# Optimization experiments

Measured on AMD Instinct MI355X. Metric: run time of the kernel, lower is better.

## Reference

```python
import jax, jax.numpy as jnp
import numpy as np

B, I, H, DEPTH = 128, 768, 768, 8        # levels 0 (root) .. 7 (leaves)
NODES = 2 ** DEPTH - 1                    # 255 nodes, heap / level order
EPS = 1e-5                                # torch LayerNorm default


def setup_inputs() -> dict:
    key = jax.random.key(0)
    ks = jax.random.split(key, 8)
    s = 0.02  # xavier-ish scale to keep gates in a sane range
    return {
        "x": jax.random.normal(ks[0], (B, NODES, I), jnp.float32),
        "Wioux": jax.random.normal(ks[1], (DEPTH, 3 * H, I), jnp.float32) * s,
        "b_ioux": jnp.zeros((DEPTH, 3 * H), jnp.float32),
        "Wiouh": jax.random.normal(ks[2], (DEPTH, 3 * H, H), jnp.float32) * s,
        "Wfx": jax.random.normal(ks[3], (DEPTH, H, I), jnp.float32) * s,
        "b_fx": jnp.ones((DEPTH, H), jnp.float32),  # fx.bias init to ones per _init_weights
        "Wfh": jax.random.normal(ks[4], (DEPTH, H, H), jnp.float32) * s,
        "b_fh": jnp.zeros((DEPTH, H), jnp.float32),
        "ln_c_g": jnp.ones((DEPTH, H), jnp.float32),
        "ln_c_b": jnp.zeros((DEPTH, H), jnp.float32),
        "ln_h_g": jnp.ones((DEPTH, H), jnp.float32),
        "ln_h_b": jnp.zeros((DEPTH, H), jnp.float32),
        "Wout": jax.random.normal(ks[5], (H, H), jnp.float32) * s,
        "b_out": jnp.zeros((H,), jnp.float32),
    }


def _ln(v, g, b):
    m = v.mean(-1, keepdims=True)
    var = ((v - m) ** 2).mean(-1, keepdims=True)
    return (v - m) / jnp.sqrt(var + EPS) * g + b


def reference(x, Wioux, b_ioux, Wiouh, Wfx, b_fx, Wfh, b_fh,
              ln_c_g, ln_c_b, ln_h_g, ln_h_b, Wout, b_out):
    """Child-Sum TreeLSTM over a complete binary tree (heap-ordered nodes),
    processed bottom-up level-by-level; depth-l nodes use parameter set l."""
    bsz = x.shape[0]
    h = None
    for l in range(DEPTH - 1, -1, -1):       # leaves -> root
        n = 2 ** l
        xs = x[:, n - 1:2 * n - 1]            # [B, n, I] inputs at level l
        iou = jnp.einsum('bni,gi->bng', xs, Wioux[l]) + b_ioux[l]
        if h is not None:
            ch_h = h.reshape(bsz, n, 2, H)    # two children per node
            iou = iou + jnp.einsum('bnh,gh->bng', ch_h.sum(2), Wiouh[l])
        i_, o_, u_ = jnp.split(iou, 3, axis=-1)
        i_ = jax.nn.sigmoid(i_)
        o_ = jax.nn.sigmoid(o_)
        u_ = jnp.tanh(u_)
        c = i_ * u_
        if h is not None:
            fxo = jnp.einsum('bni,hi->bnh', xs, Wfx[l]) + b_fx[l]
            f = jax.nn.sigmoid(fxo[:, :, None, :]
                               + jnp.einsum('bnkh,gh->bnkg', ch_h, Wfh[l]) + b_fh[l])
            # NOTE: faithful to source: f gates multiply child *hidden* states
            c = c + (f * ch_h).sum(2)
        c = _ln(c, ln_c_g[l], ln_c_b[l])
        h = o_ * jnp.tanh(c)
        h = _ln(h, ln_h_g[l], ln_h_b[l])      # dropout is identity in eval
    h_root = h[:, 0]                          # [B, H]
    return jnp.einsum('bh,gh->bg', h_root, Wout) + b_out + x[:, 0]
```

## Files before the change

kernel.cpp:

```cpp
#include <hip/hip_runtime.h>
#include <hip/hip_bf16.h>


#define Hdim 768

typedef __hip_bfloat16 bf16;
typedef __attribute__((ext_vector_type(8))) short short8;
typedef __attribute__((ext_vector_type(4))) float floatx4;

__device__ inline float b2f(unsigned short u) {
    union { unsigned int i; float f; } v; v.i = ((unsigned int)u) << 16; return v.f;
}
__device__ inline float b2f(bf16 h) { return b2f(*(unsigned short*)&h); }
__device__ inline unsigned short f2bu(float f) {
    bf16 h = __float2bfloat16(f);
    return *(unsigned short*)&h;
}
__device__ inline ushort4 cvt4(float4 v) {
    ushort4 o; o.x = f2bu(v.x); o.y = f2bu(v.y); o.z = f2bu(v.z); o.w = f2bu(v.w);
    return o;
}

__global__ __launch_bounds__(384) void conv_wcat(
    const float* __restrict__ Wioux, const float* __restrict__ Wiouh,
    const float* __restrict__ Wfx, bf16* __restrict__ W_cat)
{
    const int row = blockIdx.x;
    const int l = row / 3072;
    const int g = row % 3072;
    const int t = threadIdx.x;
    const int k2 = t << 2;
    float4 v;
    if (g < 2304) {
        const float* src = (k2 < 768)
            ? Wioux + ((long)l * 2304 + g) * 768 + k2
            : Wiouh + ((long)l * 2304 + g) * 768 + (k2 - 768);
        v = *(const float4*)src;
    } else if (k2 < 768) {
        v = *(const float4*)(Wfx + ((long)l * 768 + (g - 2304)) * 768 + k2);
    } else {
        v = make_float4(0.f, 0.f, 0.f, 0.f);
    }
    ((ushort4*)(W_cat + (long)row * 1536))[t] = cvt4(v);
}

__global__ __launch_bounds__(256) void prep_misc(
    const float* __restrict__ Wfh, const float* __restrict__ Wout,
    const float* __restrict__ b_ioux, const float* __restrict__ b_fx,
    const float* __restrict__ x,
    bf16* __restrict__ Wfh_bf, bf16* __restrict__ Wout_bf,
    float* __restrict__ b_cat, bf16* __restrict__ leafA)
{
    const int id = blockIdx.x;
    const int t = threadIdx.x;
    if (id < 4608) {
        const long i = (long)id * 256 + t;
        ((ushort4*)Wfh_bf)[i] = cvt4(((const float4*)Wfh)[i]);
    } else if (id < 5184) {
        const long i = (long)(id - 4608) * 256 + t;
        ((ushort4*)Wout_bf)[i] = cvt4(((const float4*)Wout)[i]);
    } else if (id < 5280) {
        const int i = (id - 5184) * 256 + t;
        const int l = i / 3072, g = i % 3072;
        b_cat[i] = (g < 2304) ? b_ioux[l * 2304 + g] : b_fx[l * 768 + (g - 2304)];
    } else if (t < 192) {
        const int m = id - 5280;
        const int b = m >> 7, j = m & 127;
        const float* xr = x + ((long)b * 255 + 127 + j) * Hdim;
        ((ushort4*)(leafA + (long)m * Hdim))[t] = cvt4(((const float4*)xr)[t]);
    }
}

struct GemmDesc {
    const bf16* A; int lda;
    const bf16* W; int ldw;
    const float* bias;
    void* C; int ldc; int c_fp32;
    int K; int nxb;
    const float* addv; long add_stride;
};

static inline GemmDesc mkdesc(const bf16* A, int lda, const bf16* W, int ldw,
                              const float* bias, void* C, int ldc, int c_fp32,
                              int K, int nxb, const float* addv, long add_stride) {
    GemmDesc d; d.A = A; d.lda = lda; d.W = W; d.ldw = ldw; d.bias = bias;
    d.C = C; d.ldc = ldc; d.c_fp32 = c_fp32; d.K = K; d.nxb = nxb;
    d.addv = addv; d.add_stride = add_stride; return d;
}

__global__ __launch_bounds__(256) void gemm_dual(GemmDesc da, int na, GemmDesc db)
{
    __shared__ __align__(16) bf16 As[128 * 32];
    __shared__ __align__(16) bf16 Ws[128 * 32];
    int id = blockIdx.x;
    const bool second = (id >= na);
    if (second) id -= na;
    const GemmDesc d = second ? db : da;
    const int bm = id / d.nxb, bn = id % d.nxb;

    const int t = threadIdx.x;
    const int wave = t >> 6, lane = t & 63;
    const long m_blk = (long)bm << 7;
// ... 43 lines not shown
        for (int i = 0; i < 4; i++) {
            af[i]  = *(const short8*)(AsS + (mrow + i * 16 + fm) * 32 + fk);
            bfr[i] = *(const short8*)(WsS + (ncol + i * 16 + fm) * 32 + fk);
        }
#pragma unroll
        for (int i = 0; i < 4; i++)
#pragma unroll
            for (int j = 0; j < 4; j++)
                acc[i][j] = __builtin_amdgcn_mfma_f32_16x16x32_bf16(
                    af[i], bfr[j], acc[i][j], 0, 0, 0);
        __syncthreads();
    }

    const int crow0 = (lane >> 4) << 2;
    const int ccol = lane & 15;
#pragma unroll
    for (int i = 0; i < 4; i++) {
#pragma unroll
        for (int j = 0; j < 4; j++) {
            const long col = n_blk + ncol + j * 16 + ccol;
            const float bv = d.bias ? d.bias[col] : 0.f;
#pragma unroll
            for (int r = 0; r < 4; r++) {
                const long row = m_blk + mrow + i * 16 + crow0 + r;
                float v = acc[i][j][r] + bv;
                if (d.addv) v += d.addv[row * d.add_stride + col];
                if (d.c_fp32) ((float*)d.C)[row * (long)d.ldc + col] = v;
                else ((bf16*)d.C)[row * (long)d.ldc + col] = __float2bfloat16(v);
            }
        }
    }
}

__global__ __launch_bounds__(512, 2) void gemm8_dual(GemmDesc da, int na, GemmDesc db)
{
    __shared__ __align__(16) char smem[131072];

    int id = blockIdx.x;
    int nwg = na;
    bool second = false;
    if (id >= na) { id -= na; nwg = (int)gridDim.x - na; second = true; }
    const GemmDesc d = second ? db : da;
    {
        const int q = nwg >> 3, r = nwg & 7;
        const int x = id & 7, i2 = id >> 3;
        id = (x < r ? x * (q + 1) : r * (q + 1) + (x - r) * q) + i2;
    }
    const int bm = id / d.nxb, bn = id % d.nxb;
    const int tid = threadIdx.x;
    const int w = tid >> 6, lane = tid & 63;
    const long m_blk = (long)bm << 8;
    const long n_blk = (long)bn << 8;
    const int T = d.K >> 6;

    const int colb = (((lane & 7) ^ ((lane >> 3) & 7)) << 4);
    const int rw = (w << 4) + (lane >> 3);
    const long ldaB = (long)d.lda * 2, ldwB = (long)d.ldw * 2;
    const char* gA0 = (const char*)(d.A + m_blk * d.lda) + (long)rw * ldaB + colb;
    const char* gB0 = (const char*)(d.W + n_blk * d.ldw) + (long)rw * ldwB + colb;
    const long aH = ldaB << 7, bH = ldwB << 7;
    const long a8 = ldaB << 3, b8 = ldwB << 3;
    char* lW = smem + (w << 11);

    auto stageA = [&](int tile, int buf, int half) {
        const char* g = gA0 + (half ? aH : 0) + ((long)tile << 7);
        char* l = lW + buf * 32768 + half * 16384;
        __builtin_amdgcn_global_load_lds(
            (const __attribute__((address_space(1))) unsigned int*)g,
            (__attribute__((address_space(3))) unsigned int*)l, 16, 0, 0);
        __builtin_amdgcn_global_load_lds(
            (const __attribute__((address_space(1))) unsigned int*)(g + a8),
            (__attribute__((address_space(3))) unsigned int*)(l + 1024), 16, 0, 0);
    };
    auto stageB = [&](int tile, int buf, int half) {
        const char* g = gB0 + (half ? bH : 0) + ((long)tile << 7);
        char* l = lW + 65536 + buf * 32768 + half * 16384;
        __builtin_amdgcn_global_load_lds(
            (const __attribute__((address_space(1))) unsigned int*)g,
            (__attribute__((address_space(3))) unsigned int*)l, 16, 0, 0);
        __builtin_amdgcn_global_load_lds(
            (const __attribute__((address_space(1))) unsigned int*)(g + b8),
            (__attribute__((address_space(3))) unsigned int*)(l + 1024), 16, 0, 0);
    };

    const int fm = lane & 15;
    const int fkB = (lane >> 4) << 4;
    const int sx = (lane & 7) << 4;
    const int cx0 = fkB ^ sx;
    const int cx1 = cx0 ^ 64;
    const int arow0 = ((w >> 2) << 7) + fm;
    const int brow0 = ((w & 3) << 6) + fm;

    floatx4 acc[8][4];
    const floatx4 fzero = {0.f, 0.f, 0.f, 0.f};
#pragma unroll
    for (int i = 0; i < 8; i++)
#pragma unroll
        for (int j = 0; j < 4; j++) acc[i][j] = fzero;

    stageA(0, 0, 0); stageA(0, 0, 1); stageB(0, 0, 0); stageB(0, 0, 1);
    if (T > 1) {
        stageB(1, 1, 0); stageB(1, 1, 1); stageA(1, 1, 0);
        asm volatile("s_waitcnt vmcnt(6)" ::: "memory");
    } else {
        asm volatile("s_waitcnt vmcnt(0)" ::: "memory");
    }
    __builtin_amdgcn_sched_barrier(0);
    __builtin_amdgcn_s_barrier();
    __builtin_amdgcn_sched_barrier(0);

    short8 a[4][2], b[4][2];
    for (int tt = 0; tt < T; ++tt) {
        const int buf = tt & 1;
        const char* la = smem + buf * 32768;
        const char* lb = smem + 65536 + buf * 32768;
#pragma unroll
        for (int mf = 0; mf < 4; ++mf) {
            a[mf][0] = *(const short8*)(la + ((arow0 + mf * 16) << 7) + cx0);
            a[mf][1] = *(const short8*)(la + ((arow0 + mf * 16) << 7) + cx1);
        }
#pragma unroll
        for (int nf = 0; nf < 2; ++nf) {
            b[nf][0] = *(const short8*)(lb + ((brow0 + nf * 16) << 7) + cx0);
            b[nf][1] = *(const short8*)(lb + ((brow0 + nf * 16) << 7) + cx1);
        }
        if (tt + 1 < T) stageA(tt + 1, buf ^ 1, 1);
        __builtin_amdgcn_s_barrier();
        asm volatile("s_waitcnt lgkmcnt(0)" ::: "memory");
        __builtin_amdgcn_sched_barrier(0);
        __builtin_amdgcn_s_setprio(1);
#pragma unroll
        for (int ks = 0; ks < 2; ++ks)
#pragma unroll
            for (int mf = 0; mf < 4; ++mf)
#pragma unroll
                for (int nf = 0; nf < 2; ++nf)
                    acc[mf][nf] = __builtin_amdgcn_mfma_f32_16x16x32_bf16(
                        a[mf][ks], b[nf][ks], acc[mf][nf], 0, 0, 0);
        __builtin_amdgcn_s_setprio(0);
        __builtin_amdgcn_s_barrier();
        __builtin_amdgcn_sched_barrier(0);
#pragma unroll
        for (int nf = 0; nf < 2; ++nf) {
            b[2 + nf][0] = *(const short8*)(lb + ((brow0 + (2 + nf) * 16) << 7) + cx0);
            b[2 + nf][1] = *(const short8*)(lb + ((brow0 + (2 + nf) * 16) << 7) + cx1);
        }
        __builtin_amdgcn_s_barrier();
        asm volatile("s_waitcnt lgkmcnt(0)" ::: "memory");
        __builtin_amdgcn_sched_barrier(0);
        __builtin_amdgcn_s_setprio(1);
#pragma unroll
        for (int ks = 0; ks < 2; ++ks)
#pragma unroll
            for (int mf = 0; mf < 4; ++mf)
#pragma unroll
                for (int nf = 0; nf < 2; ++nf)
                    acc[mf][2 + nf] = __builtin_amdgcn_mfma_f32_16x16x32_bf16(
                        a[mf][ks], b[2 + nf][ks], acc[mf][2 + nf], 0, 0, 0);
        __builtin_amdgcn_s_setprio(0);
        __builtin_amdgcn_s_barrier();
        __builtin_amdgcn_sched_barrier(0);
#pragma unroll
        for (int mf = 0; mf < 4; ++mf) {
            a[mf][0] = *(const short8*)(la + ((arow0 + (4 + mf) * 16) << 7) + cx0);
            a[mf][1] = *(const short8*)(la + ((arow0 + (4 + mf) * 16) << 7) + cx1);
        }
        if (tt + 2 < T) stageB(tt + 2, buf, 0);
        __builtin_amdgcn_s_barrier();
        asm volatile("s_waitcnt lgkmcnt(0)" ::: "memory");
        __builtin_amdgcn_sched_barrier(0);
        __builtin_amdgcn_s_setprio(1);
#pragma unroll
        for (int ks = 0; ks < 2; ++ks)
#pragma unroll
            for (int mf = 0; mf < 4; ++mf)
#pragma unroll
                for (int nf = 0; nf < 2; ++nf)
                    acc[4 + mf][2 + nf] = __builtin_amdgcn_mfma_f32_16x16x32_bf16(
                        a[mf][ks], b[2 + nf][ks], acc[4 + mf][2 + nf], 0, 0, 0);
        __builtin_amdgcn_s_setprio(0);
        __builtin_amdgcn_s_barrier();
        __builtin_amdgcn_sched_barrier(0);
        if (tt + 2 < T) { stageB(tt + 2, buf, 1); stageA(tt + 2, buf, 0); }
        __builtin_amdgcn_s_setprio(1);
#pragma unroll
        for (int ks = 0; ks < 2; ++ks)
#pragma unroll
            for (int mf = 0; mf < 4; ++mf)
#pragma unroll
                for (int nf = 0; nf < 2; ++nf)
                    acc[4 + mf][nf] = __builtin_amdgcn_mfma_f32_16x16x32_bf16(
                        a[mf][ks], b[nf][ks], acc[4 + mf][nf], 0, 0, 0);
        __builtin_amdgcn_s_setprio(0);
        if (tt + 1 < T) {
            if (tt + 2 < T) asm volatile("s_waitcnt vmcnt(6)" ::: "memory");
            else            asm volatile("s_waitcnt vmcnt(0)" ::: "memory");
            __builtin_amdgcn_sched_barrier(0);
            __builtin_amdgcn_s_barrier();
            __builtin_amdgcn_sched_barrier(0);
        }
    }

    const int crow = (lane >> 4) << 2;
    const int ccol = lane & 15;
    const long row0 = m_blk + ((long)(w >> 2) << 7);
    const long col0 = n_blk + ((w & 3) << 6);
#pragma unroll
    for (int mf = 0; mf < 8; ++mf) {
#pragma unroll
        for (int nf = 0; nf < 4; ++nf) {
            const long col = col0 + nf * 16 + ccol;
            const float bv = d.bias ? d.bias[col] : 0.f;
#pragma unroll
            for (int r = 0; r < 4; ++r) {
                const long row = row0 + mf * 16 + crow + r;
                const float v = acc[mf][nf][r] + bv;
                if (d.c_fp32) ((float*)d.C)[row * (long)d.ldc + col] = v;
                else ((bf16*)d.C)[row * (long)d.ldc + col] = __float2bfloat16(v);
            }
        }
    }
}

__device__ inline float sigf(float x) { return 1.f / (1.f + __expf(-x)); }
__device__ inline float tanh_fast(float x) { return 2.f / (1.f + __expf(-2.f * x)) - 1.f; }

__device__ inline void block_reduce4(float& a, float& b, float& c, float& d,
                                     float* s) {
#pragma unroll
    for (int off = 32; off > 0; off >>= 1) {
        a += __shfl_down(a, off, 64);
        b += __shfl_down(b, off, 64);
        c += __shfl_down(c, off, 64);
        d += __shfl_down(d, off, 64);
    }
    const int lane = threadIdx.x & 63, w = threadIdx.x >> 6;
    __syncthreads();
    if (lane == 0) { s[w] = a; s[w + 4] = b; s[w + 8] = c; s[w + 12] = d; }
    __syncthreads();
    a = s[0] + s[1] + s[2] + s[3];
    b = s[4] + s[5] + s[6] + s[7];
    c = s[8] + s[9] + s[10] + s[11];
    d = s[12] + s[13] + s[14] + s[15];
}

__global__ __launch_bounds__(256) void pointwise_pair(
    const bf16* __restrict__ C, int ldc,
    const bf16* __restrict__ fhb,
    const bf16* __restrict__ hprev2,
    const float* __restrict__ x,
    const float* __restrict__ bfh,
    const float* __restrict__ gc, const float* __restrict__ bc,
    const float* __restrict__ gh, const float* __restrict__ bh,
    bf16* __restrict__ hout,
    bf16* __restrict__ Anext,
    int m0, int lp)
{
    __shared__ float sred[16];
    const int pl = blockIdx.x;
    const bf16* cr0 = C + (long)(2 * pl) * ldc;
    const bf16* cr1 = cr0 + ldc;
    float c0v[3], c1v[3], o0v[3], o1v[3], h0v[3], h1v[3];
    float s0 = 0.f, q0 = 0.f, s1 = 0.f, q1 = 0.f;
#pragma unroll
    for (int tI = 0; tI < 3; tI++) {
        const int j = threadIdx.x + tI * 256;
        const float i0 = sigf(b2f(cr0[j]));
        const float i1 = sigf(b2f(cr1[j]));
        o0v[tI] = b2f(cr0[Hdim + j]);
        o1v[tI] = b2f(cr1[Hdim + j]);
        float c0 = i0 * tanh_fast(b2f(cr0[2 * Hdim + j]));
        float c1 = i1 * tanh_fast(b2f(cr1[2 * Hdim + j]));
        if (fhb) {
            const float bfhj = bfh[j];
            const float fx0 = b2f(cr0[3 * Hdim + j]);
            const float fx1 = b2f(cr1[3 * Hdim + j]);
            const long base = (long)(4 * pl) * Hdim + j;
            const float f00 = sigf(fx0 + b2f(fhb[base]) + bfhj);
            const float f01 = sigf(fx0 + b2f(fhb[base + Hdim]) + bfhj);
            const float f10 = sigf(fx1 + b2f(fhb[base + 2 * Hdim]) + bfhj);
            const float f11 = sigf(fx1 + b2f(fhb[base + 3 * Hdim]) + bfhj);
            c0 += f00 * b2f(hprev2[base]) + f01 * b2f(hprev2[base + Hdim]);
            c1 += f10 * b2f(hprev2[base + 2 * Hdim]) + f11 * b2f(hprev2[base + 3 * Hdim]);
        }
        c0v[tI] = c0; c1v[tI] = c1;
        s0 += c0; q0 += c0 * c0; s1 += c1; q1 += c1 * c1;
    }
    block_reduce4(s0, q0, s1, q1, sred);
    const float m0c = s0 / Hdim, m1c = s1 / Hdim;
    const float r0c = rsqrtf(q0 / Hdim - m0c * m0c + 1e-5f);
    const float r1c = rsqrtf(q1 / Hdim - m1c * m1c + 1e-5f);
    float hs0 = 0.f, hq0 = 0.f, hs1 = 0.f, hq1 = 0.f;
#pragma unroll
    for (int tI = 0; tI < 3; tI++) {
        const int j = threadIdx.x + tI * 256;
        const float cn0 = (c0v[tI] - m0c) * r0c * gc[j] + bc[j];
        const float cn1 = (c1v[tI] - m1c) * r1c * gc[j] + bc[j];
        const float h0 = sigf(o0v[tI]) * tanh_fast(cn0);
        const float h1 = sigf(o1v[tI]) * tanh_fast(cn1);
        h0v[tI] = h0; h1v[tI] = h1;
        hs0 += h0; hq0 += h0 * h0; hs1 += h1; hq1 += h1 * h1;
    }
    block_reduce4(hs0, hq0, hs1, hq1, sred);
    const float mh0 = hs0 / Hdim, mh1 = hs1 / Hdim;
    const float rh0 = rsqrtf(hq0 / Hdim - mh0 * mh0 + 1e-5f);
    const float rh1 = rsqrtf(hq1 / Hdim - mh1 * mh1 + 1e-5f);

    const int pg = m0 / 2 + pl;
    const int b = pg >> lp;
    const int jn = pg & ((1 << lp) - 1);
    const float* xr = x + ((long)b * 255 + (1 << lp) - 1 + jn) * Hdim;
    bf16* arow = Anext + (long)pg * 1536;
#pragma unroll
    for (int tI = 0; tI < 3; tI++) {
        const int j = threadIdx.x + tI * 256;
        const float h0 = (h0v[tI] - mh0) * rh0 * gh[j] + bh[j];
        const float h1 = (h1v[tI] - mh1) * rh1 * gh[j] + bh[j];
        hout[(long)(2 * pl) * Hdim + j] = __float2bfloat16(h0);
        hout[(long)(2 * pl + 1) * Hdim + j] = __float2bfloat16(h1);
        arow[768 + j] = __float2bfloat16(h0 + h1);
        arow[j] = __float2bfloat16(xr[j]);
    }
}

__global__ __launch_bounds__(256) void pointwise_root(
    const bf16* __restrict__ C, int ldc,
    const bf16* __restrict__ fhb, const bf16* __restrict__ hprev,
    const float* __restrict__ bfh,
    const float* __restrict__ gc, const float* __restrict__ bc,
    const float* __restrict__ gh, const float* __restrict__ bh,
    bf16* __restrict__ hout)
{
    __shared__ float sred[16];
    const int m = blockIdx.x;
    const bf16* cr = C + (long)m * ldc;
    float cv[3], ov[3], hv[3];
    float ssum = 0.f, ssq = 0.f, d0 = 0.f, d1 = 0.f;
#pragma unroll
    for (int tI = 0; tI < 3; tI++) {
        const int j = threadIdx.x + tI * 256;
        const float i_ = sigf(b2f(cr[j]));
        ov[tI] = b2f(cr[Hdim + j]);
        float c = i_ * tanh_fast(b2f(cr[2 * Hdim + j]));
        const float fx = b2f(cr[3 * Hdim + j]);
        const float bfhj = bfh[j];
        const long base = (long)(2 * m) * Hdim + j;
        const float f0 = sigf(fx + b2f(fhb[base]) + bfhj);
        const float f1 = sigf(fx + b2f(fhb[base + Hdim]) + bfhj);
        c += f0 * b2f(hprev[base]) + f1 * b2f(hprev[base + Hdim]);
        cv[tI] = c; ssum += c; ssq += c * c;
    }
    block_reduce4(ssum, ssq, d0, d1, sred);
    const float mean = ssum / Hdim;
    const float rstd = rsqrtf(ssq / Hdim - mean * mean + 1e-5f);
    float hs = 0.f, hq = 0.f;
#pragma unroll
    for (int tI = 0; tI < 3; tI++) {
        const int j = threadIdx.x + tI * 256;
        const float cn = (cv[tI] - mean) * rstd * gc[j] + bc[j];
        const float h = sigf(ov[tI]) * tanh_fast(cn);
        hv[tI] = h; hs += h; hq += h * h;
    }
    d0 = 0.f; d1 = 0.f;
    block_reduce4(hs, hq, d0, d1, sred);
    const float mh = hs / Hdim;
    const float rh = rsqrtf(hq / Hdim - mh * mh + 1e-5f);
#pragma unroll
    for (int tI = 0; tI < 3; tI++) {
        const int j = threadIdx.x + tI * 256;
        hout[(long)m * Hdim + j] = __float2bfloat16((hv[tI] - mh) * rh * gh[j] + bh[j]);
    }
}

extern "C" void kernel_launch(void* const* d_in, const int* in_sizes, int n_in,
                              void* d_out, int out_size, void* d_ws, size_t ws_size,
                              hipStream_t stream) {
    (void)in_sizes; (void)n_in; (void)out_size; (void)ws_size;
    const float* x      = (const float*)d_in[0];
    const float* Wioux  = (const float*)d_in[1];
    const float* b_ioux = (const float*)d_in[2];
    const float* Wiouh  = (const float*)d_in[3];
    const float* Wfx    = (const float*)d_in[4];
    const float* b_fx   = (const float*)d_in[5];
    const float* Wfh    = (const float*)d_in[6];
    const float* b_fh   = (const float*)d_in[7];
    const float* ln_c_g = (const float*)d_in[8];
    const float* ln_c_b = (const float*)d_in[9];
    const float* ln_h_g = (const float*)d_in[10];
    const float* ln_h_b = (const float*)d_in[11];
    const float* Wout   = (const float*)d_in[12];
    const float* b_out  = (const float*)d_in[13];
    float* out = (float*)d_out;

    char* p = (char*)d_ws;
    bf16* W_cat   = (bf16*)p; p += 8L * 3072 * 1536 * 2;
    bf16* Wfh_bf  = (bf16*)p; p += 8L * 768 * 768 * 2;
    bf16* Wout_bf = (bf16*)p; p += 768L * 768 * 2;
    float* b_cat  = (float*)p; p += 8L * 3072 * 4;
    bf16* leafA   = (bf16*)p; p += 16384L * 768 * 2;
    bf16* A6      = (bf16*)p; p += 8192L * 1536 * 2;
    bf16* A5      = (bf16*)p; p += 4096L * 1536 * 2;
    bf16* Cbuf    = (bf16*)p; p += 4096L * 3072 * 2;
    bf16* hA      = (bf16*)p; p += 16384L * 768 * 2;
    bf16* hB      = (bf16*)p; p += 8192L * 768 * 2;
    bf16* fhb     = leafA;
    bf16* Cleaf   = A5;

    conv_wcat<<<8 * 3072, 384, 0, stream>>>(Wioux, Wiouh, Wfx, W_cat);
    prep_misc<<<5280 + 16384, 256, 0, stream>>>(
        Wfh, Wout, b_ioux, b_fx, x, Wfh_bf, Wout_bf, b_cat, leafA);

    GemmDesc dummy = mkdesc(nullptr, 0, nullptr, 0, nullptr, nullptr, 0, 0, 0, 1,
                            nullptr, 0);

    for (int c = 0; c < 2; c++) {
        const int m0 = c * 8192;
        GemmDesc dl = mkdesc(leafA + (long)m0 * 768, 768,
                             W_cat + 7L * 3072 * 1536, 1536, b_cat + 7 * 3072,
                             Cleaf, 2304, 0, 768, 9, nullptr, 0);
        gemm8_dual<<<9 * 32, 512, 0, stream>>>(dl, 9 * 32, dummy);
        pointwise_pair<<<4096, 256, 0, stream>>>(
            Cleaf, 2304, nullptr, nullptr, x, nullptr,
            ln_c_g + 7 * Hdim, ln_c_b + 7 * Hdim, ln_h_g + 7 * Hdim, ln_h_b + 7 * Hdim,
            hA + (long)m0 * Hdim, A6, m0, 6);
    }

    const int CH = 4096;
    bf16* hp = hA; bf16* hc = hB;
    bf16* Acur = A6; bf16* Anxt = A5;
    for (int l = 6; l >= 1; l--) {
        const int M = 128 << l;
        const int Mc = (M < CH) ? M : CH;
        const int nch = M / Mc;
        for (int c = 0; c < nch; c++) {
            const int m0 = c * Mc;
            GemmDesc diou = mkdesc(Acur + (long)m0 * 1536, 1536,
                                   W_cat + (long)l * 3072 * 1536, 1536,
                                   b_cat + l * 3072, Cbuf, 3072, 0, 1536, 12,
                                   nullptr, 0);
            const int na = 12 * (Mc / 256);
            if (c == 0) {
                GemmDesc dfh = mkdesc(hp, 768,
                                      Wfh_bf + (long)l * 768 * 768, 768, nullptr,
                                      fhb, 768, 0, 768, 3, nullptr, 0);
                const int nb = 3 * (2 * M / 256);
                gemm8_dual<<<na + nb, 512, 0, stream>>>(diou, na, dfh);
            } else {
                gemm8_dual<<<na, 512, 0, stream>>>(diou, na, dummy);
            }
            pointwise_pair<<<Mc / 2, 256, 0, stream>>>(
                Cbuf, 3072, fhb + (long)2 * m0 * Hdim, hp + (long)2 * m0 * Hdim,
                x, b_fh + l * Hdim,
                ln_c_g + l * Hdim, ln_c_b + l * Hdim, ln_h_g + l * Hdim, ln_h_b + l * Hdim,
                hc + (long)m0 * Hdim, Anxt, m0, l - 1);
        }
        bf16* t1 = hp; hp = hc; hc = t1;
        bf16* t2 = Acur; Acur = Anxt; Anxt = t2;
    }

    {
        GemmDesc diou = mkdesc(Acur, 1536, W_cat, 1536, b_cat, Cbuf, 3072, 0,
                               1536, 24, nullptr, 0);
        GemmDesc dfh = mkdesc(hp, 768, Wfh_bf, 768, nullptr, fhb, 768, 0,
                              768, 6, nullptr, 0);
        gemm_dual<<<24 + 12, 256, 0, stream>>>(diou, 24, dfh);
        pointwise_root<<<128, 256, 0, stream>>>(
            Cbuf, 3072, fhb, hp, b_fh,
            ln_c_g, ln_c_b, ln_h_g, ln_h_b, hc);
    }

    {
        GemmDesc dout = mkdesc(hc, 768, Wout_bf, 768, b_out, out, 768, 1,
                               768, 6, x, 255L * 768);
        gemm_dual<<<6, 256, 0, stream>>>(dout, 6, dummy);
    }
}
```

Measured before the change: 1.003 ms.

## Persistent atomic-scheduled GEMM, vectorized pointwise, rebalanced chunks and small-level kernel

The 256x256 MFMA GEMM becomes persistent: at most 256 workgroups take tile indices from a global atomic counter, and the counters are zeroed in prep_misc. Leaf-level work is split into three chunks instead of two, the fh GEMM is chunked together with the iou GEMM, and levels below 5 switch to the smaller-tile gemm_dual kernel. The pointwise kernels move to 4-wide bf16 vector loads and stores with 192 active threads. The aim is to cut tail-wave imbalance and launch granularity on small levels, at the cost of atomic and extra barrier overhead per tile.

```diff
diff --git a/kernel.cpp b/kernel.cpp
--- a/kernel.cpp
+++ b/kernel.cpp
@@ -19,6 +19,14 @@
 __device__ inline ushort4 cvt4(float4 v) {
     ushort4 o; o.x = f2bu(v.x); o.y = f2bu(v.y); o.z = f2bu(v.z); o.w = f2bu(v.w);
     return o;
+}
+__device__ inline void ld4(const bf16* p, float* o) {
+    ushort4 u = *(const ushort4*)p;
+    o[0] = b2f(u.x); o[1] = b2f(u.y); o[2] = b2f(u.z); o[3] = b2f(u.w);
+}
+__device__ inline void st4(bf16* p, const float* v) {
+    ushort4 u; u.x = f2bu(v[0]); u.y = f2bu(v[1]); u.z = f2bu(v[2]); u.w = f2bu(v[3]);
+    *(ushort4*)p = u;
 }
 
 __global__ __launch_bounds__(384) void conv_wcat(
@@ -49,7 +57,8 @@
     const float* __restrict__ b_ioux, const float* __restrict__ b_fx,
     const float* __restrict__ x,
     bf16* __restrict__ Wfh_bf, bf16* __restrict__ Wout_bf,
-    float* __restrict__ b_cat, bf16* __restrict__ leafA)
+    float* __restrict__ b_cat, bf16* __restrict__ leafA,
+    unsigned int* __restrict__ ctrs)
 {
     const int id = blockIdx.x;
     const int t = threadIdx.x;
@@ -63,11 +72,15 @@
         const int i = (id - 5184) * 256 + t;
         const int l = i / 3072, g = i % 3072;
         b_cat[i] = (g < 2304) ? b_ioux[l * 2304 + g] : b_fx[l * 768 + (g - 2304)];
-    } else if (t < 192) {
-        const int m = id - 5280;
-        const int b = m >> 7, j = m & 127;
-        const float* xr = x + ((long)b * 255 + 127 + j) * Hdim;
-        ((ushort4*)(leafA + (long)m * Hdim))[t] = cvt4(((const float4*)xr)[t]);
+    } else if (id < 21664) {
+        if (t < 192) {
+            const int m = id - 5280;
+            const int b = m >> 7, j = m & 127;
+            const float* xr = x + ((long)b * 255 + 127 + j) * Hdim;
+            ((ushort4*)(leafA + (long)m * Hdim))[t] = cvt4(((const float4*)xr)[t]);
+        }
+    } else {
+        if (t < 16) ctrs[t] = 0;
     }
 }
 
@@ -177,57 +190,17 @@
     }
 }
 
-__global__ __launch_bounds__(512, 2) void gemm8_dual(GemmDesc da, int na, GemmDesc db)
+__global__ __launch_bounds__(512, 2) void gemm8_dual(
+    GemmDesc da, int na, GemmDesc db, int ntot, unsigned int* __restrict__ ctr)
 {
     __shared__ __align__(16) char smem[131072];
-
-    int id = blockIdx.x;
-    int nwg = na;
-    bool second = false;
-    if (id >= na) { id -= na; nwg = (int)gridDim.x - na; second = true; }
-    const GemmDesc d = second ? db : da;
-    {
-        const int q = nwg >> 3, r = nwg & 7;
-        const int x = id & 7, i2 = id >> 3;
-        id = (x < r ? x * (q + 1) : r * (q + 1) + (x - r) * q) + i2;
-    }
-    const int bm = id / d.nxb, bn = id % d.nxb;
+    __shared__ int sjob;
+
     const int tid = threadIdx.x;
     const int w = tid >> 6, lane = tid & 63;
-    const long m_blk = (long)bm << 8;
-    const long n_blk = (long)bn << 8;
-    const int T = d.K >> 6;
 
     const int colb = (((lane & 7) ^ ((lane >> 3) & 7)) << 4);
     const int rw = (w << 4) + (lane >> 3);
-    const long ldaB = (long)d.lda * 2, ldwB = (long)d.ldw * 2;
-    const char* gA0 = (const char*)(d.A + m_blk * d.lda) + (long)rw * ldaB + colb;
-    const char* gB0 = (const char*)(d.W + n_blk * d.ldw) + (long)rw * ldwB + colb;
-    const long aH = ldaB << 7, bH = ldwB << 7;
-    const long a8 = ldaB << 3, b8 = ldwB << 3;
-    char* lW = smem + (w << 11);
-
-    auto stageA = [&](int tile, int buf, int half) {
-        const char* g = gA0 + (half ? aH : 0) + ((long)tile << 7);
-        char* l = lW + buf * 32768 + half * 16384;
-        __builtin_amdgcn_global_load_lds(
-            (const __attribute__((address_space(1))) unsigned int*)g,
-            (__attribute__((address_space(3))) unsigned int*)l, 16, 0, 0);
-        __builtin_amdgcn_global_load_lds(
-            (const __attribute__((address_space(1))) unsigned int*)(g + a8),
-            (__attribute__((address_space(3))) unsigned int*)(l + 1024), 16, 0, 0);
-    };
-    auto stageB = [&](int tile, int buf, int half) {
-        const char* g = gB0 + (half ? bH : 0) + ((long)tile << 7);
-        char* l = lW + 65536 + buf * 32768 + half * 16384;
-        __builtin_amdgcn_global_load_lds(
-            (const __attribute__((address_space(1))) unsigned int*)g,
-            (__attribute__((address_space(3))) unsigned int*)l, 16, 0, 0);
-        __builtin_amdgcn_global_load_lds(
-            (const __attribute__((address_space(1))) unsigned int*)(g + b8),
-            (__attribute__((address_space(3))) unsigned int*)(l + 1024), 16, 0, 0);
-    };
-
     const int fm = lane & 15;
     const int fkB = (lane >> 4) << 4;
     const int sx = (lane & 7) << 4;
@@ -235,133 +208,176 @@
     const int cx1 = cx0 ^ 64;
     const int arow0 = ((w >> 2) << 7) + fm;
     const int brow0 = ((w & 3) << 6) + fm;
-
-    floatx4 acc[8][4];
-    const floatx4 fzero = {0.f, 0.f, 0.f, 0.f};
-#pragma unroll
-    for (int i = 0; i < 8; i++)
-#pragma unroll
-        for (int j = 0; j < 4; j++) acc[i][j] = fzero;
-
-    stageA(0, 0, 0); stageA(0, 0, 1); stageB(0, 0, 0); stageB(0, 0, 1);
-    if (T > 1) {
-        stageB(1, 1, 0); stageB(1, 1, 1); stageA(1, 1, 0);
-        asm volatile("s_waitcnt vmcnt(6)" ::: "memory");
-    } else {
-        asm volatile("s_waitcnt vmcnt(0)" ::: "memory");
-    }
-    __builtin_amdgcn_sched_barrier(0);
-    __builtin_amdgcn_s_barrier();
-    __builtin_amdgcn_sched_barrier(0);
-
-    short8 a[4][2], b[4][2];
-    for (int tt = 0; tt < T; ++tt) {
-        const int buf = tt & 1;
-        const char* la = smem + buf * 32768;
-        const char* lb = smem + 65536 + buf * 32768;
-#pragma unroll
-        for (int mf = 0; mf < 4; ++mf) {
-            a[mf][0] = *(const short8*)(la + ((arow0 + mf * 16) << 7) + cx0);
-            a[mf][1] = *(const short8*)(la + ((arow0 + mf * 16) << 7) + cx1);
-        }
-#pragma unroll
-        for (int nf = 0; nf < 2; ++nf) {
-            b[nf][0] = *(const short8*)(lb + ((brow0 + nf * 16) << 7) + cx0);
-            b[nf][1] = *(const short8*)(lb + ((brow0 + nf * 16) << 7) + cx1);
-        }
-        if (tt + 1 < T) stageA(tt + 1, buf ^ 1, 1);
-        __builtin_amdgcn_s_barrier();
-        asm volatile("s_waitcnt lgkmcnt(0)" ::: "memory");
+    char* lW = smem + (w << 11);
+
+    for (;;) {
+        __syncthreads();
+        if (tid == 0) sjob = (int)atomicAdd(ctr, 1u);
+        __syncthreads();
+        int id = sjob;
+        if (id >= ntot) return;
+        const bool second = (id >= na);
+        if (second) id -= na;
+        const GemmDesc d = second ? db : da;
+        const int bm = id / d.nxb, bn = id % d.nxb;
+        const long m_blk = (long)bm << 8;
+        const long n_blk = (long)bn << 8;
+        const int T = d.K >> 6;
+
+        const long ldaB = (long)d.lda * 2, ldwB = (long)d.ldw * 2;
+        const char* gA0 = (const char*)(d.A + m_blk * d.lda) + (long)rw * ldaB + colb;
+        const char* gB0 = (const char*)(d.W + n_blk * d.ldw) + (long)rw * ldwB + colb;
+        const long aH = ldaB << 7, bH = ldwB << 7;
+        const long a8 = ldaB << 3, b8 = ldwB << 3;
+
+        auto stageA = [&](int tile, int buf, int half) {
+            const char* g = gA0 + (half ? aH : 0) + ((long)tile << 7);
+            char* l = lW + buf * 32768 + half * 16384;
+            __builtin_amdgcn_global_load_lds(
+                (const __attribute__((address_space(1))) unsigned int*)g,
+                (__attribute__((address_space(3))) unsigned int*)l, 16, 0, 0);
+            __builtin_amdgcn_global_load_lds(
+                (const __attribute__((address_space(1))) unsigned int*)(g + a8),
+                (__attribute__((address_space(3))) unsigned int*)(l + 1024), 16, 0, 0);
+        };
+        auto stageB = [&](int tile, int buf, int half) {
+            const char* g = gB0 + (half ? bH : 0) + ((long)tile << 7);
+            char* l = lW + 65536 + buf * 32768 + half * 16384;
+            __builtin_amdgcn_global_load_lds(
+                (const __attribute__((address_space(1))) unsigned int*)g,
+                (__attribute__((address_space(3))) unsigned int*)l, 16, 0, 0);
+            __builtin_amdgcn_global_load_lds(
+                (const __attribute__((address_space(1))) unsigned int*)(g + b8),
+                (__attribute__((address_space(3))) unsigned int*)(l + 1024), 16, 0, 0);
+        };
+
+        floatx4 acc[8][4];
+        const floatx4 fzero = {0.f, 0.f, 0.f, 0.f};
+#pragma unroll
+        for (int i = 0; i < 8; i++)
+#pragma unroll
+            for (int j = 0; j < 4; j++) acc[i][j] = fzero;
+
+        stageA(0, 0, 0); stageA(0, 0, 1); stageB(0, 0, 0); stageB(0, 0, 1);
+        if (T > 1) {
+            stageB(1, 1, 0); stageB(1, 1, 1); stageA(1, 1, 0);
+            asm volatile("s_waitcnt vmcnt(6)" ::: "memory");
+        } else {
+            asm volatile("s_waitcnt vmcnt(0)" ::: "memory");
+        }
         __builtin_amdgcn_sched_barrier(0);
-        __builtin_amdgcn_s_setprio(1);
-#pragma unroll
-        for (int ks = 0; ks < 2; ++ks)
-#pragma unroll
-            for (int mf = 0; mf < 4; ++mf)
-#pragma unroll
-                for (int nf = 0; nf < 2; ++nf)
-                    acc[mf][nf] = __builtin_amdgcn_mfma_f32_16x16x32_bf16(
-                        a[mf][ks], b[nf][ks], acc[mf][nf], 0, 0, 0);
-        __builtin_amdgcn_s_setprio(0);
         __builtin_amdgcn_s_barrier();
         __builtin_amdgcn_sched_barrier(0);
-#pragma unroll
-        for (int nf = 0; nf < 2; ++nf) {
-            b[2 + nf][0] = *(const short8*)(lb + ((brow0 + (2 + nf) * 16) << 7) + cx0);
-            b[2 + nf][1] = *(const short8*)(lb + ((brow0 + (2 + nf) * 16) << 7) + cx1);
-        }
-        __builtin_amdgcn_s_barrier();
-        asm volatile("s_waitcnt lgkmcnt(0)" ::: "memory");
-        __builtin_amdgcn_sched_barrier(0);
-        __builtin_amdgcn_s_setprio(1);
-#pragma unroll
-        for (int ks = 0; ks < 2; ++ks)
-#pragma unroll
-            for (int mf = 0; mf < 4; ++mf)
-#pragma unroll
-                for (int nf = 0; nf < 2; ++nf)
-                    acc[mf][2 + nf] = __builtin_amdgcn_mfma_f32_16x16x32_bf16(
-                        a[mf][ks], b[2 + nf][ks], acc[mf][2 + nf], 0, 0, 0);
-        __builtin_amdgcn_s_setprio(0);
-        __builtin_amdgcn_s_barrier();
-        __builtin_amdgcn_sched_barrier(0);
-#pragma unroll
-        for (int mf = 0; mf < 4; ++mf) {
-            a[mf][0] = *(const short8*)(la + ((arow0 + (4 + mf) * 16) << 7) + cx0);
-            a[mf][1] = *(const short8*)(la + ((arow0 + (4 + mf) * 16) << 7) + cx1);
-        }
-        if (tt + 2 < T) stageB(tt + 2, buf, 0);
-        __builtin_amdgcn_s_barrier();
-        asm volatile("s_waitcnt lgkmcnt(0)" ::: "memory");
-        __builtin_amdgcn_sched_barrier(0);
-        __builtin_amdgcn_s_setprio(1);
-#pragma unroll
-        for (int ks = 0; ks < 2; ++ks)
-#pragma unroll
-            for (int mf = 0; mf < 4; ++mf)
-#pragma unroll
-                for (int nf = 0; nf < 2; ++nf)
-                    acc[4 + mf][2 + nf] = __builtin_amdgcn_mfma_f32_16x16x32_bf16(
-                        a[mf][ks], b[2 + nf][ks], acc[4 + mf][2 + nf], 0, 0, 0);
-        __builtin_amdgcn_s_setprio(0);
-        __builtin_amdgcn_s_barrier();
-        __builtin_amdgcn_sched_barrier(0);
-        if (tt + 2 < T) { stageB(tt + 2, buf, 1); stageA(tt + 2, buf, 0); }
-        __builtin_amdgcn_s_setprio(1);
-#pragma unroll
-        for (int ks = 0; ks < 2; ++ks)
-#pragma unroll
-            for (int mf = 0; mf < 4; ++mf)
-#pragma unroll
-                for (int nf = 0; nf < 2; ++nf)
-                    acc[4 + mf][nf] = __builtin_amdgcn_mfma_f32_16x16x32_bf16(
-                        a[mf][ks], b[nf][ks], acc[4 + mf][nf], 0, 0, 0);
-        __builtin_amdgcn_s_setprio(0);
-        if (tt + 1 < T) {
-            if (tt + 2 < T) asm volatile("s_waitcnt vmcnt(6)" ::: "memory");
-            else            asm volatile("s_waitcnt vmcnt(0)" ::: "memory");
+
+        short8 a[4][2], b[4][2];
+        for (int tt = 0; tt < T; ++tt) {
+            const int buf = tt & 1;
+            const char* la = smem + buf * 32768;
+            const char* lb = smem + 65536 + buf * 32768;
+#pragma unroll
+            for (int mf = 0; mf < 4; ++mf) {
+                a[mf][0] = *(const short8*)(la + ((arow0 + mf * 16) << 7) + cx0);
+                a[mf][1] = *(const short8*)(la + ((arow0 + mf * 16) << 7) + cx1);
+            }
+#pragma unroll
+            for (int nf = 0; nf < 2; ++nf) {
+                b[nf][0] = *(const short8*)(lb + ((brow0 + nf * 16) << 7) + cx0);
+                b[nf][1] = *(const short8*)(lb + ((brow0 + nf * 16) << 7) + cx1);
+            }
+            if (tt + 1 < T) stageA(tt + 1, buf ^ 1, 1);
+            __builtin_amdgcn_s_barrier();
+            asm volatile("s_waitcnt lgkmcnt(0)" ::: "memory");
             __builtin_amdgcn_sched_barrier(0);
+            __builtin_amdgcn_s_setprio(1);
+#pragma unroll
+            for (int ks = 0; ks < 2; ++ks)
+#pragma unroll
+                for (int mf = 0; mf < 4; ++mf)
+#pragma unroll
+                    for (int nf = 0; nf < 2; ++nf)
+                        acc[mf][nf] = __builtin_amdgcn_mfma_f32_16x16x32_bf16(
+                            a[mf][ks], b[nf][ks], acc[mf][nf], 0, 0, 0);
+            __builtin_amdgcn_s_setprio(0);
             __builtin_amdgcn_s_barrier();
             __builtin_amdgcn_sched_barrier(0);
-        }
-    }
-
-    const int crow = (lane >> 4) << 2;
-    const int ccol = lane & 15;
-    const long row0 = m_blk + ((long)(w >> 2) << 7);
-    const long col0 = n_blk + ((w & 3) << 6);
-#pragma unroll
-    for (int mf = 0; mf < 8; ++mf) {
-#pragma unroll
-        for (int nf = 0; nf < 4; ++nf) {
-            const long col = col0 + nf * 16 + ccol;
-            const float bv = d.bias ? d.bias[col] : 0.f;
-#pragma unroll
-            for (int r = 0; r < 4; ++r) {
-                const long row = row0 + mf * 16 + crow + r;
-                const float v = acc[mf][nf][r] + bv;
-                if (d.c_fp32) ((float*)d.C)[row * (long)d.ldc + col] = v;
-                else ((bf16*)d.C)[row * (long)d.ldc + col] = __float2bfloat16(v);
+#pragma unroll
+            for (int nf = 0; nf < 2; ++nf) {
+                b[2 + nf][0] = *(const short8*)(lb + ((brow0 + (2 + nf) * 16) << 7) + cx0);
+                b[2 + nf][1] = *(const short8*)(lb + ((brow0 + (2 + nf) * 16) << 7) + cx1);
+            }
+            __builtin_amdgcn_s_barrier();
+            asm volatile("s_waitcnt lgkmcnt(0)" ::: "memory");
+            __builtin_amdgcn_sched_barrier(0);
+            __builtin_amdgcn_s_setprio(1);
+#pragma unroll
+            for (int ks = 0; ks < 2; ++ks)
+#pragma unroll
+                for (int mf = 0; mf < 4; ++mf)
+#pragma unroll
+                    for (int nf = 0; nf < 2; ++nf)
+                        acc[mf][2 + nf] = __builtin_amdgcn_mfma_f32_16x16x32_bf16(
+                            a[mf][ks], b[2 + nf][ks], acc[mf][2 + nf], 0, 0, 0);
+            __builtin_amdgcn_s_setprio(0);
+            __builtin_amdgcn_s_barrier();
+            __builtin_amdgcn_sched_barrier(0);
+#pragma unroll
+            for (int mf = 0; mf < 4; ++mf) {
+                a[mf][0] = *(const short8*)(la + ((arow0 + (4 + mf) * 16) << 7) + cx0);
+                a[mf][1] = *(const short8*)(la + ((arow0 + (4 + mf) * 16) << 7) + cx1);
+            }
+            if (tt + 2 < T) stageB(tt + 2, buf, 0);
+            __builtin_amdgcn_s_barrier();
+            asm volatile("s_waitcnt lgkmcnt(0)" ::: "memory");
+            __builtin_amdgcn_sched_barrier(0);
+            __builtin_amdgcn_s_setprio(1);
+#pragma unroll
+            for (int ks = 0; ks < 2; ++ks)
+#pragma unroll
+                for (int mf = 0; mf < 4; ++mf)
+#pragma unroll
+                    for (int nf = 0; nf < 2; ++nf)
+                        acc[4 + mf][2 + nf] = __builtin_amdgcn_mfma_f32_16x16x32_bf16(
+                            a[mf][ks], b[2 + nf][ks], acc[4 + mf][2 + nf], 0, 0, 0);
+            __builtin_amdgcn_s_setprio(0);
+            __builtin_amdgcn_s_barrier();
+            __builtin_amdgcn_sched_barrier(0);
+            if (tt + 2 < T) { stageB(tt + 2, buf, 1); stageA(tt + 2, buf, 0); }
+            __builtin_amdgcn_s_setprio(1);
+#pragma unroll
+            for (int ks = 0; ks < 2; ++ks)
+#pragma unroll
+                for (int mf = 0; mf < 4; ++mf)
+#pragma unroll
+                    for (int nf = 0; nf < 2; ++nf)
+                        acc[4 + mf][nf] = __builtin_amdgcn_mfma_f32_16x16x32_bf16(
+                            a[mf][ks], b[nf][ks], acc[4 + mf][nf], 0, 0, 0);
+            __builtin_amdgcn_s_setprio(0);
+            if (tt + 1 < T) {
+                if (tt + 2 < T) asm volatile("s_waitcnt vmcnt(6)" ::: "memory");
+                else            asm volatile("s_waitcnt vmcnt(0)" ::: "memory");
+                __builtin_amdgcn_sched_barrier(0);
+                __builtin_amdgcn_s_barrier();
+                __builtin_amdgcn_sched_barrier(0);
+            }
+        }
+
+        const int crow = (lane >> 4) << 2;
+        const int ccol = lane & 15;
+        const long row0 = m_blk + ((long)(w >> 2) << 7);
+        const long col0 = n_blk + ((w & 3) << 6);
+#pragma unroll
+        for (int mf = 0; mf < 8; ++mf) {
+#pragma unroll
+            for (int nf = 0; nf < 4; ++nf) {
+                const long col = col0 + nf * 16 + ccol;
+                const float bv = d.bias ? d.bias[col] : 0.f;
+#pragma unroll
+                for (int r = 0; r < 4; ++r) {
+                    const long row = row0 + mf * 16 + crow + r;
+                    const float v = acc[mf][nf][r] + bv;
+                    if (d.c_fp32) ((float*)d.C)[row * (long)d.ldc + col] = v;
+                    else ((bf16*)d.C)[row * (long)d.ldc + col] = __float2bfloat16(v);
+                }
             }
         }
     }
@@ -403,68 +419,94 @@
 {
     __shared__ float sred[16];
     const int pl = blockIdx.x;
+    const int t = threadIdx.x;
+    const bool act = t < 192;
+    const int j = t << 2;
     const bf16* cr0 = C + (long)(2 * pl) * ldc;
     const bf16* cr1 = cr0 + ldc;
-    float c0v[3], c1v[3], o0v[3], o1v[3], h0v[3], h1v[3];
+    float c0v[4], c1v[4], o0v[4], o1v[4], h0v[4], h1v[4];
     float s0 = 0.f, q0 = 0.f, s1 = 0.f, q1 = 0.f;
-#pragma unroll
-    for (int tI = 0; tI < 3; tI++) {
-        const int j = threadIdx.x + tI * 256;
-        const float i0 = sigf(b2f(cr0[j]));
-        const float i1 = sigf(b2f(cr1[j]));
-        o0v[tI] = b2f(cr0[Hdim + j]);
-        o1v[tI] = b2f(cr1[Hdim + j]);
-        float c0 = i0 * tanh_fast(b2f(cr0[2 * Hdim + j]));
-        float c1 = i1 * tanh_fast(b2f(cr1[2 * Hdim + j]));
+    if (act) {
+        float i0[4], i1[4], u0[4], u1[4];
+        ld4(cr0 + j, i0); ld4(cr1 + j, i1);
+        ld4(cr0 + Hdim + j, o0v); ld4(cr1 + Hdim + j, o1v);
+        ld4(cr0 + 2 * Hdim + j, u0); ld4(cr1 + 2 * Hdim + j, u1);
         if (fhb) {
-            const float bfhj = bfh[j];
-            const float fx0 = b2f(cr0[3 * Hdim + j]);
-            const float fx1 = b2f(cr1[3 * Hdim + j]);
+            float fx0[4], fx1[4], fb0[4], fb1[4], fb2[4], fb3[4];
+            float hp0[4], hp1[4], hp2[4], hp3[4];
+            ld4(cr0 + 3 * Hdim + j, fx0); ld4(cr1 + 3 * Hdim + j, fx1);
             const long base = (long)(4 * pl) * Hdim + j;
-            const float f00 = sigf(fx0 + b2f(fhb[base]) + bfhj);
-            const float f01 = sigf(fx0 + b2f(fhb[base + Hdim]) + bfhj);
-            const float f10 = sigf(fx1 + b2f(fhb[base + 2 * Hdim]) + bfhj);
-            const float f11 = sigf(fx1 + b2f(fhb[base + 3 * Hdim]) + bfhj);
-            c0 += f00 * b2f(hprev2[base]) + f01 * b2f(hprev2[base + Hdim]);
-            c1 += f10 * b2f(hprev2[base + 2 * Hdim]) + f11 * b2f(hprev2[base + 3 * Hdim]);
-        }
-        c0v[tI] = c0; c1v[tI] = c1;
-        s0 += c0; q0 += c0 * c0; s1 += c1; q1 += c1 * c1;
+            ld4(fhb + base, fb0); ld4(fhb + base + Hdim, fb1);
+            ld4(fhb + base + 2 * Hdim, fb2); ld4(fhb + base + 3 * Hdim, fb3);
+            ld4(hprev2 + base, hp0); ld4(hprev2 + base + Hdim, hp1);
+            ld4(hprev2 + base + 2 * Hdim, hp2); ld4(hprev2 + base + 3 * Hdim, hp3);
+            const float4 bf4 = *(const float4*)(bfh + j);
+#pragma unroll
+            for (int q = 0; q < 4; q++) {
+                const float bq = (&bf4.x)[q];
+                float c0 = sigf(i0[q]) * tanh_fast(u0[q]);
+                float c1 = sigf(i1[q]) * tanh_fast(u1[q]);
+                c0 += sigf(fx0[q] + fb0[q] + bq) * hp0[q]
+                    + sigf(fx0[q] + fb1[q] + bq) * hp1[q];
+                c1 += sigf(fx1[q] + fb2[q] + bq) * hp2[q]
+                    + sigf(fx1[q] + fb3[q] + bq) * hp3[q];
+                c0v[q] = c0; c1v[q] = c1;
+                s0 += c0; q0 += c0 * c0; s1 += c1; q1 += c1 * c1;
+            }
+        } else {
+#pragma unroll
+            for (int q = 0; q < 4; q++) {
+                const float c0 = sigf(i0[q]) * tanh_fast(u0[q]);
+                const float c1 = sigf(i1[q]) * tanh_fast(u1[q]);
+                c0v[q] = c0; c1v[q] = c1;
+                s0 += c0; q0 += c0 * c0; s1 += c1; q1 += c1 * c1;
+            }
+        }
     }
     block_reduce4(s0, q0, s1, q1, sred);
     const float m0c = s0 / Hdim, m1c = s1 / Hdim;
     const float r0c = rsqrtf(q0 / Hdim - m0c * m0c + 1e-5f);
     const float r1c = rsqrtf(q1 / Hdim - m1c * m1c + 1e-5f);
     float hs0 = 0.f, hq0 = 0.f, hs1 = 0.f, hq1 = 0.f;
-#pragma unroll
-    for (int tI = 0; tI < 3; tI++) {
-        const int j = threadIdx.x + tI * 256;
-        const float cn0 = (c0v[tI] - m0c) * r0c * gc[j] + bc[j];
-        const float cn1 = (c1v[tI] - m1c) * r1c * gc[j] + bc[j];
-        const float h0 = sigf(o0v[tI]) * tanh_fast(cn0);
-        const float h1 = sigf(o1v[tI]) * tanh_fast(cn1);
-        h0v[tI] = h0; h1v[tI] = h1;
-        hs0 += h0; hq0 += h0 * h0; hs1 += h1; hq1 += h1 * h1;
+    if (act) {
+        const float4 gc4 = *(const float4*)(gc + j);
+        const float4 bc4 = *(const float4*)(bc + j);
+#pragma unroll
+        for (int q = 0; q < 4; q++) {
+            const float cn0 = (c0v[q] - m0c) * r0c * (&gc4.x)[q] + (&bc4.x)[q];
+            const float cn1 = (c1v[q] - m1c) * r1c * (&gc4.x)[q] + (&bc4.x)[q];
+            const float h0 = sigf(o0v[q]) * tanh_fast(cn0);
+            const float h1 = sigf(o1v[q]) * tanh_fast(cn1);
+            h0v[q] = h0; h1v[q] = h1;
+            hs0 += h0; hq0 += h0 * h0; hs1 += h1; hq1 += h1 * h1;
+        }
     }
     block_reduce4(hs0, hq0, hs1, hq1, sred);
     const float mh0 = hs0 / Hdim, mh1 = hs1 / Hdim;
     const float rh0 = rsqrtf(hq0 / Hdim - mh0 * mh0 + 1e-5f);
     const float rh1 = rsqrtf(hq1 / Hdim - mh1 * mh1 + 1e-5f);
 
-    const int pg = m0 / 2 + pl;
-    const int b = pg >> lp;
-    const int jn = pg & ((1 << lp) - 1);
-    const float* xr = x + ((long)b * 255 + (1 << lp) - 1 + jn) * Hdim;
-    bf16* arow = Anext + (long)pg * 1536;
-#pragma unroll
-    for (int tI = 0; tI < 3; tI++) {
-        const int j = threadIdx.x + tI * 256;
-        const float h0 = (h0v[tI] - mh0) * rh0 * gh[j] + bh[j];
-        const float h1 = (h1v[tI] - mh1) * rh1 * gh[j] + bh[j];
-        hout[(long)(2 * pl) * Hdim + j] = __float2bfloat16(h0);
-        hout[(long)(2 * pl + 1) * Hdim + j] = __float2bfloat16(h1);
-        arow[768 + j] = __float2bfloat16(h0 + h1);
-        arow[j] = __float2bfloat16(xr[j]);
+    if (act) {
+        const int pg = m0 / 2 + pl;
+        const int b = pg >> lp;
+        const int jn = pg & ((1 << lp) - 1);
+        const float* xr = x + ((long)b * 255 + (1 << lp) - 1 + jn) * Hdim;
+        bf16* arow = Anext + (long)pg * 1536;
+        const float4 gh4 = *(const float4*)(gh + j);
+        const float4 bh4 = *(const float4*)(bh + j);
+        const float4 xr4 = *(const float4*)(xr + j);
+        float hh0[4], hh1[4], ha[4], xs[4];
+#pragma unroll
+        for (int q = 0; q < 4; q++) {
+            hh0[q] = (h0v[q] - mh0) * rh0 * (&gh4.x)[q] + (&bh4.x)[q];
+            hh1[q] = (h1v[q] - mh1) * rh1 * (&gh4.x)[q] + (&bh4.x)[q];
+            ha[q] = hh0[q] + hh1[q];
+            xs[q] = (&xr4.x)[q];
+        }
+        st4(hout + (long)(2 * pl) * Hdim + j, hh0);
+        st4(hout + (long)(2 * pl + 1) * Hdim + j, hh1);
+        st4(arow + 768 + j, ha);
+        st4(arow + j, xs);
     }
 }
 
@@ -478,42 +520,55 @@
 {
     __shared__ float sred[16];
     const int m = blockIdx.x;
+    const int t = threadIdx.x;
+    const bool act = t < 192;
+    const int j = t << 2;
     const bf16* cr = C + (long)m * ldc;
-    float cv[3], ov[3], hv[3];
+    float cv[4], ov[4], hv[4];
     float ssum = 0.f, ssq = 0.f, d0 = 0.f, d1 = 0.f;
-#pragma unroll
-    for (int tI = 0; tI < 3; tI++) {
-        const int j = threadIdx.x + tI * 256;
-        const float i_ = sigf(b2f(cr[j]));
-        ov[tI] = b2f(cr[Hdim + j]);
-        float c = i_ * tanh_fast(b2f(cr[2 * Hdim + j]));
-        const float fx = b2f(cr[3 * Hdim + j]);
-        const float bfhj = bfh[j];
+    if (act) {
+        float iv[4], uv[4], fx[4], fb0[4], fb1[4], hp0[4], hp1[4];
+        ld4(cr + j, iv); ld4(cr + Hdim + j, ov); ld4(cr + 2 * Hdim + j, uv);
+        ld4(cr + 3 * Hdim + j, fx);
         const long base = (long)(2 * m) * Hdim + j;
-        const float f0 = sigf(fx + b2f(fhb[base]) + bfhj);
-        const float f1 = sigf(fx + b2f(fhb[base + Hdim]) + bfhj);
-        c += f0 * b2f(hprev[base]) + f1 * b2f(hprev[base + Hdim]);
-        cv[tI] = c; ssum += c; ssq += c * c;
+        ld4(fhb + base, fb0); ld4(fhb + base + Hdim, fb1);
+        ld4(hprev + base, hp0); ld4(hprev + base + Hdim, hp1);
+        const float4 bf4 = *(const float4*)(bfh + j);
+#pragma unroll
+        for (int q = 0; q < 4; q++) {
+            const float bq = (&bf4.x)[q];
+            float c = sigf(iv[q]) * tanh_fast(uv[q]);
+            c += sigf(fx[q] + fb0[q] + bq) * hp0[q]
+               + sigf(fx[q] + fb1[q] + bq) * hp1[q];
+            cv[q] = c; ssum += c; ssq += c * c;
+        }
     }
     block_reduce4(ssum, ssq, d0, d1, sred);
     const float mean = ssum / Hdim;
     const float rstd = rsqrtf(ssq / Hdim - mean * mean + 1e-5f);
     float hs = 0.f, hq = 0.f;
-#pragma unroll
-    for (int tI = 0; tI < 3; tI++) {
-        const int j = threadIdx.x + tI * 256;
-        const float cn = (cv[tI] - mean) * rstd * gc[j] + bc[j];
-        const float h = sigf(ov[tI]) * tanh_fast(cn);
-        hv[tI] = h; hs += h; hq += h * h;
+    if (act) {
+        const float4 gc4 = *(const float4*)(gc + j);
+        const float4 bc4 = *(const float4*)(bc + j);
+#pragma unroll
+        for (int q = 0; q < 4; q++) {
+            const float cn = (cv[q] - mean) * rstd * (&gc4.x)[q] + (&bc4.x)[q];
+            const float h = sigf(ov[q]) * tanh_fast(cn);
+            hv[q] = h; hs += h; hq += h * h;
+        }
     }
     d0 = 0.f; d1 = 0.f;
     block_reduce4(hs, hq, d0, d1, sred);
     const float mh = hs / Hdim;
     const float rh = rsqrtf(hq / Hdim - mh * mh + 1e-5f);
-#pragma unroll
-    for (int tI = 0; tI < 3; tI++) {
-        const int j = threadIdx.x + tI * 256;
-        hout[(long)m * Hdim + j] = __float2bfloat16((hv[tI] - mh) * rh * gh[j] + bh[j]);
+    if (act) {
+        const float4 gh4 = *(const float4*)(gh + j);
+        const float4 bh4 = *(const float4*)(bh + j);
+        float hh[4];
+#pragma unroll
+        for (int q = 0; q < 4; q++)
+            hh[q] = (hv[q] - mh) * rh * (&gh4.x)[q] + (&bh4.x)[q];
+        st4(hout + (long)m * Hdim + j, hh);
     }
 }
 
@@ -548,26 +603,34 @@
     bf16* Cbuf    = (bf16*)p; p += 4096L * 3072 * 2;
     bf16* hA      = (bf16*)p; p += 16384L * 768 * 2;
     bf16* hB      = (bf16*)p; p += 8192L * 768 * 2;
+    unsigned int* ctrs = (unsigned int*)p; p += 64;
     bf16* fhb     = leafA;
     bf16* Cleaf   = A5;
 
     conv_wcat<<<8 * 3072, 384, 0, stream>>>(Wioux, Wiouh, Wfx, W_cat);
-    prep_misc<<<5280 + 16384, 256, 0, stream>>>(
-        Wfh, Wout, b_ioux, b_fx, x, Wfh_bf, Wout_bf, b_cat, leafA);
+    prep_misc<<<5280 + 16384 + 1, 256, 0, stream>>>(
+        Wfh, Wout, b_ioux, b_fx, x, Wfh_bf, Wout_bf, b_cat, leafA, ctrs);
 
     GemmDesc dummy = mkdesc(nullptr, 0, nullptr, 0, nullptr, nullptr, 0, 0, 0, 1,
                             nullptr, 0);
-
-    for (int c = 0; c < 2; c++) {
-        const int m0 = c * 8192;
-        GemmDesc dl = mkdesc(leafA + (long)m0 * 768, 768,
-                             W_cat + 7L * 3072 * 1536, 1536, b_cat + 7 * 3072,
-                             Cleaf, 2304, 0, 768, 9, nullptr, 0);
-        gemm8_dual<<<9 * 32, 512, 0, stream>>>(dl, 9 * 32, dummy);
-        pointwise_pair<<<4096, 256, 0, stream>>>(
-            Cleaf, 2304, nullptr, nullptr, x, nullptr,
-            ln_c_g + 7 * Hdim, ln_c_b + 7 * Hdim, ln_h_g + 7 * Hdim, ln_h_b + 7 * Hdim,
-            hA + (long)m0 * Hdim, A6, m0, 6);
+    int kc = 0;
+
+    {
+        const int cm0[3] = {0, 5632, 11264};
+        const int cmc[3] = {5632, 5632, 5120};
+        for (int c = 0; c < 3; c++) {
+            const int m0 = cm0[c], Mc = cmc[c];
+            GemmDesc dl = mkdesc(leafA + (long)m0 * 768, 768,
+                                 W_cat + 7L * 3072 * 1536, 1536, b_cat + 7 * 3072,
+                                 Cleaf, 2304, 0, 768, 9, nullptr, 0);
+            const int ntot = (Mc / 256) * 9;
+            gemm8_dual<<<(ntot < 256 ? ntot : 256), 512, 0, stream>>>(
+                dl, ntot, dummy, ntot, ctrs + kc++);
+            pointwise_pair<<<Mc / 2, 256, 0, stream>>>(
+                Cleaf, 2304, nullptr, nullptr, x, nullptr,
+                ln_c_g + 7 * Hdim, ln_c_b + 7 * Hdim, ln_h_g + 7 * Hdim, ln_h_b + 7 * Hdim,
+                hA + (long)m0 * Hdim, A6, m0, 6);
+        }
     }
 
     const int CH = 4096;
@@ -579,23 +642,33 @@
         const int nch = M / Mc;
         for (int c = 0; c < nch; c++) {
             const int m0 = c * Mc;
-            GemmDesc diou = mkdesc(Acur + (long)m0 * 1536, 1536,
-                                   W_cat + (long)l * 3072 * 1536, 1536,
-                                   b_cat + l * 3072, Cbuf, 3072, 0, 1536, 12,
-                                   nullptr, 0);
-            const int na = 12 * (Mc / 256);
-            if (c == 0) {
-                GemmDesc dfh = mkdesc(hp, 768,
+            if (l >= 5) {
+                GemmDesc diou = mkdesc(Acur + (long)m0 * 1536, 1536,
+                                       W_cat + (long)l * 3072 * 1536, 1536,
+                                       b_cat + l * 3072, Cbuf, 3072, 0, 1536, 12,
+                                       nullptr, 0);
+                GemmDesc dfh = mkdesc(hp + (long)2 * m0 * Hdim, 768,
                                       Wfh_bf + (long)l * 768 * 768, 768, nullptr,
                                       fhb, 768, 0, 768, 3, nullptr, 0);
-                const int nb = 3 * (2 * M / 256);
-                gemm8_dual<<<na + nb, 512, 0, stream>>>(diou, na, dfh);
+                const int na = 12 * (Mc / 256);
+                const int nb = 3 * (2 * Mc / 256);
+                const int ntot = na + nb;
+                gemm8_dual<<<(ntot < 256 ? ntot : 256), 512, 0, stream>>>(
+                    diou, na, dfh, ntot, ctrs + kc++);
             } else {
-                gemm8_dual<<<na, 512, 0, stream>>>(diou, na, dummy);
+                GemmDesc diou = mkdesc(Acur + (long)m0 * 1536, 1536,
+                                       W_cat + (long)l * 3072 * 1536, 1536,
+                                       b_cat + l * 3072, Cbuf, 3072, 0, 1536, 24,
+                                       nullptr, 0);
+                GemmDesc dfh = mkdesc(hp + (long)2 * m0 * Hdim, 768,
+                                      Wfh_bf + (long)l * 768 * 768, 768, nullptr,
+                                      fhb, 768, 0, 768, 6, nullptr, 0);
+                const int na = 24 * (Mc / 128);
+                const int nb = 6 * (2 * Mc / 128);
+                gemm_dual<<<na + nb, 256, 0, stream>>>(diou, na, dfh);
             }
             pointwise_pair<<<Mc / 2, 256, 0, stream>>>(
-                Cbuf, 3072, fhb + (long)2 * m0 * Hdim, hp + (long)2 * m0 * Hdim,
-                x, b_fh + l * Hdim,
+                Cbuf, 3072, fhb, hp + (long)2 * m0 * Hdim, x, b_fh + l * Hdim,
                 ln_c_g + l * Hdim, ln_c_b + l * Hdim, ln_h_g + l * Hdim, ln_h_b + l * Hdim,
                 hc + (long)m0 * Hdim, Anxt, m0, l - 1);
         }
```

After: 990.0 us. No clear change (-1.3%).
